# Optimization experiments

Measured on AMD Instinct MI355X. Metric: run time of the kernel, lower is better.

## Reference

```python
import jax, jax.numpy as jnp
import numpy as np

TOP_K = 2


def setup_inputs() -> dict:
    key = jax.random.key(0)
    k0, k1, k2, k3 = jax.random.split(key, 4)
    N, D, O, E = 131072, 512, 512, 16
    H = D // 4  # gate hidden: gate_input_size // 4
    x = jax.random.normal(k0, (N, D), dtype=jnp.float32)
    # gate MLP params (task_bh=0 gate; Linear weights stored as [in, out])
    Wg1 = jax.random.normal(k1, (D, H), dtype=jnp.float32) / np.sqrt(D).astype(np.float32)
    bg1 = jnp.zeros((H,), jnp.float32)
    Wg2 = jax.random.normal(k2, (H, E), dtype=jnp.float32) * 0.02
    bg2 = jnp.zeros((E,), jnp.float32)
    # per-expert Linear(D, O) weights stacked [E, D, O]
    We = jax.random.normal(k3, (E, D, O), dtype=jnp.float32) / np.sqrt(D).astype(np.float32)
    be = jnp.zeros((E, O), jnp.float32)
    return {"x": x, "Wg1": Wg1, "bg1": bg1, "Wg2": Wg2, "bg2": bg2,
            "We": We, "be": be, "task_bh": 0}


def reference(x, Wg1, bg1, Wg2, bg2, We, be, task_bh):
    # --- top_k_gating (noisy_gating=False path) ---
    h = jax.nn.gelu(x @ Wg1 + bg1, approximate=False)  # nn.GELU default is exact erf
    logits = h @ Wg2 + bg2                              # [N, E]
    probs = jax.nn.softmax(logits, axis=1) + 1e-4       # [N, E]
    top_g, top_i = jax.lax.top_k(probs, TOP_K)          # [N, K]
    N, E = probs.shape
    # dense gate matrix: zeros.scatter(1, top_k_indices, top_k_gates)
    gates = jnp.zeros_like(probs).at[jnp.arange(N)[:, None], top_i].set(top_g)
    # --- dispatch / per-expert GEMM / combine ---
    # Equivalent to: gather tokens per expert, expert Linear, scale by gate,
    # scatter-add back. Since gates[n, e] == 0 for unselected experts, the
    # combined output equals sum_e gates[:, e] * (x @ We[e] + be[e]).
    def body(acc, ewb):
        W_e, b_e, g_e = ewb                      # [D,O], [O], [N]
        return acc + g_e[:, None] * (x @ W_e + b_e), None
    init = jnp.zeros((N, We.shape[2]), x.dtype)
    out, _ = jax.lax.scan(body, init, (We, be, gates.T))
    return out
```

## Files before the change

kernel.cpp:

```cpp
#include <hip/hip_runtime.h>
#include <cstdint>
#include <math.h>


#define NTOK 131072
#define DDIM 512

typedef short  bf16x8 __attribute__((ext_vector_type(8)));
typedef float  f32x4  __attribute__((ext_vector_type(4)));

__device__ __forceinline__ ushort f2bf(float f){
  uint u = __float_as_uint(f);
  u += 0x7fffu + ((u >> 16) & 1u);
  return (ushort)(u >> 16);
}
__device__ __forceinline__ float bf2f(ushort h){ return __uint_as_float(((uint)h) << 16); }

__device__ __forceinline__ void load_lds16(const void* g, void* l){
  __builtin_amdgcn_global_load_lds(
      (const __attribute__((address_space(1))) void*)(uintptr_t)g,
      (__attribute__((address_space(3))) void*)(uintptr_t)l, 16, 0, 0);
}

__device__ __forceinline__ f32x4 MFMA(bf16x8 a, bf16x8 b, f32x4 c){
  return __builtin_amdgcn_mfma_f32_16x16x32_bf16(a, b, c, 0, 0, 0);
}

__device__ __forceinline__ bf16x8 readF64(const char* buf, int r, int q){
  return *(const bf16x8*)(buf + r*128 + ((q ^ (r & 7)) << 4));
}
__device__ __forceinline__ bf16x8 readF32c(const char* buf, int r, int q){
  return *(const bf16x8*)(buf + r*64 + ((q ^ (r & 3)) << 4));
}

__device__ __forceinline__ void stageB32(const ushort* grow, char* lds, int tid){
  const char* gb = (const char*)grow;
  #pragma unroll
  for (int i = 0; i < 2; ++i){
    int lin = i*4096 + tid*16;
    int r = lin >> 6;
    int g = (lin >> 4) & 3;
    load_lds16(gb + r*1024 + ((g ^ (r & 3)) << 4), lds + i*4096 + ((tid >> 6) << 10));
  }
}

__device__ __forceinline__ void pack8(const float* fv, uint* ph, uint* pl){
  #pragma unroll
  for (int q=0;q<4;++q){
    float f0 = fv[2*q], f1 = fv[2*q+1];
    ushort h0 = f2bf(f0), h1 = f2bf(f1);
    ushort s0 = f2bf(f0 - bf2f(h0)), s1 = f2bf(f1 - bf2f(h1));
    ph[q] = (uint)h0 | ((uint)h1 << 16);
    pl[q] = (uint)s0 | ((uint)s1 << 16);
  }
}
__device__ __forceinline__ void writeA2p(char* hbuf, char* lbuf, int ar, int acq,
                                         const uint* ph, const uint* pl){
  int off = ar*64 + ((acq ^ (ar & 3)) << 4);
  *(uint4*)(hbuf + off) = make_uint4(ph[0],ph[1],ph[2],ph[3]);
  *(uint4*)(lbuf + off) = make_uint4(pl[0],pl[1],pl[2],pl[3]);
}

__global__ void kconv(const float* __restrict__ We, const float* __restrict__ Wg1,
                      ushort* __restrict__ Wt, ushort* __restrict__ W1h, ushort* __restrict__ W1l){
  __shared__ float sh[64*65];
  int bx = blockIdx.x, tid = threadIdx.x;
  if (bx < 1024){
    int e = bx >> 6, dt = (bx >> 3) & 7, ot = bx & 7;
    const float* src = We + (size_t)e*262144 + (size_t)dt*64*512 + ot*64;
    #pragma unroll
    for (int it=0; it<16; ++it){ int idx = it*256+tid; int dl = idx>>6, ol = idx&63;
      sh[dl*65+ol] = src[dl*512+ol]; }
    __syncthreads();
    ushort* dst = Wt + (size_t)e*262144 + (size_t)ot*64*512 + dt*64;
    #pragma unroll
    for (int it=0; it<16; ++it){ int idx = it*256+tid; int ol = idx>>6, dl = idx&63;
      dst[(size_t)ol*512+dl] = f2bf(sh[dl*65+ol]); }
  } else {
    int q = bx - 1024;
    int dt = q >> 1, ht = q & 1;
    const float* src = Wg1 + (size_t)dt*64*128 + ht*64;
    #pragma unroll
    for (int it=0; it<16; ++it){ int idx = it*256+tid; int dl = idx>>6, ol = idx&63;
      sh[dl*65+ol] = src[dl*128+ol]; }
    __syncthreads();
    #pragma unroll
    for (int it=0; it<16; ++it){ int idx = it*256+tid; int ol = idx>>6, dl = idx&63;
      float wv = sh[dl*65+ol];
      ushort hi = f2bf(wv);
      ushort lo = f2bf(wv - bf2f(hi));
      size_t o = (size_t)(ht*64+ol)*512 + dt*64+dl;
      W1h[o] = hi; W1l[o] = lo; }
  }
}

__global__ __launch_bounds__(256) void kgate(
    const float* __restrict__ x, const ushort* __restrict__ W1h, const ushort* __restrict__ W1l,
    const float* __restrict__ bg1, const float* __restrict__ Wg2, const float* __restrict__ bg2,
    ushort* __restrict__ xbf,
    int2* __restrict__ gate_e, float2* __restrict__ gate_g,
    int* __restrict__ refine_cnt, int* __restrict__ refine_list, int* __restrict__ counts)
{
  __shared__ __align__(16) char sm[49152];
  const int BOFF = 16384;
  int tid = threadIdx.x, bid = blockIdx.x;
  int lane = tid & 63, w = tid >> 6, wm = w >> 1, wn = w & 1;
  int t0 = bid * 64;
  int ar = tid >> 2, acq = tid & 3;
  const float* xrow = x + (size_t)(t0 + ar) * DDIM;
  char* xbfb = (char*)xbf;
  f32x4 acc[2][4];
  #pragma unroll
  for (int n=0;n<4;++n){
    float bb = bg1[wn*64 + n*16 + (lane & 15)];
    f32x4 z = {bb, bb, bb, bb};
    acc[0][n] = z; acc[1][n] = z;
  }
  stageB32(W1h, sm + BOFF, tid);
  stageB32(W1l, sm + BOFF + 8192, tid);
  {
    float fv[8];
    *(float4*)&fv[0] = *(const float4*)(xrow + acq*8);
    *(float4*)&fv[4] = *(const float4*)(xrow + acq*8 + 4);
    uint ph[4], pl[4];
    pack8(fv, ph, pl);
    if (xbf) *(uint4*)(xbfb + (size_t)(t0+ar)*1024 + acq*16) = make_uint4(ph[0],ph[1],ph[2],ph[3]);
    writeA2p(sm, sm + 4096, ar, acq, ph, pl);
  }
  for (int ks = 0; ks < 16; ++ks){
    int b = ks & 1;
    asm volatile("s_waitcnt vmcnt(0)" ::: "memory");
    __syncthreads();
    uint ph[4], pl[4];
    if (ks < 15){
      int k2 = ks + 1, b2 = k2 & 1;
      stageB32(W1h + k2*32, sm + BOFF + b2*16384, tid);
      stageB32(W1l + k2*32, sm + BOFF + b2*16384 + 8192, tid);
      float fv[8];
      *(float4*)&fv[0] = *(const float4*)(xrow + k2*32 + acq*8);
      *(float4*)&fv[4] = *(const float4*)(xrow + k2*32 + acq*8 + 4);
      pack8(fv, ph, pl);
      if (xbf) *(uint4*)(xbfb + (size_t)(t0+ar)*1024 + k2*64 + acq*16) = make_uint4(ph[0],ph[1],ph[2],ph[3]);
    }
    const char* Ah = sm + b*8192;
    const char* Al = Ah + 4096;
    const char* Bh = sm + BOFF + b*16384;
    const char* Bl = Bh + 8192;
    bf16x8 ah[2], alv[2], bh[4], blv[4];
    #pragma unroll
    for (int m=0;m<2;++m){
      int r = wm*32 + m*16 + (lane & 15);
      ah[m]  = readF32c(Ah, r, lane >> 4);
      alv[m] = readF32c(Al, r, lane >> 4);
    }
    #pragma unroll
    for (int n=0;n<4;++n){
      int r = wn*64 + n*16 + (lane & 15);
      bh[n]  = readF32c(Bh, r, lane >> 4);
      blv[n] = readF32c(Bl, r, lane >> 4);
    }
    #pragma unroll
    for (int m=0;m<2;++m)
      #pragma unroll
      for (int n=0;n<4;++n){
        acc[m][n] = MFMA(ah[m],  bh[n],  acc[m][n]);
        acc[m][n] = MFMA(ah[m],  blv[n], acc[m][n]);
        acc[m][n] = MFMA(alv[m], bh[n],  acc[m][n]);
      }
    if (ks < 15){
      int b2 = (ks + 1) & 1;
      writeA2p(sm + b2*8192, sm + b2*8192 + 4096, ar, acq, ph, pl);
    }
  }
  __syncthreads();
  float* hl = (float*)sm;
  #pragma unroll
  for (int m=0;m<2;++m)
    #pragma unroll
    for (int n=0;n<4;++n)
      #pragma unroll
      for (int j=0;j<4;++j){
        int row = wm*32 + m*16 + ((lane >> 4) << 2) + j;
        int col = wn*64 + n*16 + (lane & 15);
        float uv = acc[m][n][j];
        hl[row*132 + col] = 0.5f * uv * (1.0f + erff(uv * 0.70710678118654752f));
      }
  __syncthreads();
  {
    int tt = tid >> 2, cc = tid & 3;
    float4 bb = *(const float4*)(bg2 + cc*4);
    float l0 = bb.x, l1 = bb.y, l2 = bb.z, l3 = bb.w;
    const float* hrow = hl + tt*132;
    #pragma unroll 8
    for (int i = 0; i < 128; ++i){
      float hv = hrow[i];
      float4 wv = *(const float4*)(Wg2 + i*16 + cc*4);
      l0 += hv*wv.x; l1 += hv*wv.y; l2 += hv*wv.z; l3 += hv*wv.w;
    }
    float* ll = (float*)(sm + 33792);
    *(float4*)(ll + tt*16 + cc*4) = make_float4(l0, l1, l2, l3);
  }
  int* hist = (int*)(sm + 40960);
  hist[tid] = 0;
  __syncthreads();
  if (tid < 64){
    int t = t0 + tid;
    const float* l = (const float*)(sm + 33792) + tid*16;
    float b1 = -1e30f, b2 = -1e30f, b3 = -1e30f; int e1 = 0, e2 = 0;
    #pragma unroll
    for (int e = 0; e < 16; ++e){
      float v = l[e];
      if (v > b1){ b3 = b2; b2 = b1; e2 = e1; b1 = v; e1 = e; }
      else if (v > b2){ b3 = b2; b2 = v; e2 = e; }
      else if (v > b3){ b3 = v; }
    }
    double s = 0.0;
    #pragma unroll
    for (int e = 0; e < 16; ++e) s += exp((double)l[e] - (double)b1);
    double inv = 1.0 / s;
    gate_e[t] = make_int2(e1, e2);
    gate_g[t] = make_float2((float)(inv + 1e-4), (float)(exp((double)b2 - (double)b1) * inv + 1e-4));
    if (b2 - b3 < 2e-4f){
      int pos = atomicAdd(refine_cnt, 1);
      refine_list[pos] = t;
    }
    int pa = min(e1, e2), pb = max(e1, e2);
    atomicAdd(&hist[pa*16 + pb], 1);
  }
  __syncthreads();
  if (hist[tid]) atomicAdd(&counts[tid], hist[tid]);
}

__global__ __launch_bounds__(128) void krefine(
    const float* __restrict__ x, const float* __restrict__ Wg1, const float* __restrict__ bg1,
    const float* __restrict__ Wg2, const float* __restrict__ bg2,
    const int* __restrict__ refine_cnt, const int* __restrict__ refine_list,
    int2* __restrict__ gate_e, float2* __restrict__ gate_g, int* __restrict__ counts)
{
  __shared__ float  xs[512];
  __shared__ double hd[128];
  __shared__ double ld[16];
  int tid = threadIdx.x;
  int rc = *refine_cnt;
  for (int i = blockIdx.x; i < rc; i += gridDim.x){
    __syncthreads();
    int t = refine_list[i];
    *(float4*)(xs + tid*4) = *(const float4*)(x + (size_t)t*DDIM + tid*4);
    __syncthreads();
    double a = (double)bg1[tid];
    for (int d = 0; d < 512; ++d) a += (double)xs[d] * (double)Wg1[d*128 + tid];
    hd[tid] = 0.5 * a * (1.0 + erf(a * 0.70710678118654752440));
    __syncthreads();
    if (tid < 16){
      double s = (double)bg2[tid];
      for (int k = 0; k < 128; ++k) s += hd[k] * (double)Wg2[k*16 + tid];
      ld[tid] = s;
    }
    __syncthreads();
    if (tid == 0){
      int2 olde = gate_e[t];
      double b1 = -1e300, b2 = -1e300; int e1 = 0, e2 = 0;
      for (int e = 0; e < 16; ++e){
        double v = ld[e];
        if (v > b1){ b2 = b1; e2 = e1; b1 = v; e1 = e; }
        else if (v > b2){ b2 = v; e2 = e; }
      }
      double s = 0.0;
      for (int e = 0; e < 16; ++e) s += exp(ld[e] - b1);
      double inv = 1.0 / s;
      int oldp = min(olde.x, olde.y)*16 + max(olde.x, olde.y);
      int newp = min(e1, e2)*16 + max(e1, e2);
      if (oldp != newp){ atomicSub(&counts[oldp], 1); atomicAdd(&counts[newp], 1); }
      gate_e[t] = make_int2(e1, e2);
      gate_g[t] = make_float2((float)(inv + 1e-4), (float)(exp(b2 - b1) * inv + 1e-4));
    }
  }
}

__global__ void kscan(const int* __restrict__ counts, int* __restrict__ bases,
                      int* __restrict__ tile_pair, int* __restrict__ tile_row0, int* __restrict__ ntiles){
  int l = threadIdx.x;
  int4 c = *(const int4*)(counts + l*4);
  int s = c.x + c.y + c.z + c.w;
  int ps = s;
  #pragma unroll
  for (int d = 1; d < 64; d <<= 1){ int v = __shfl_up(ps, d); if (l >= d) ps += v; }
  int ex = ps - s;
  bases[4*l+0] = ex;
  bases[4*l+1] = ex + c.x;
  bases[4*l+2] = ex + c.x + c.y;
  bases[4*l+3] = ex + c.x + c.y + c.z;
  if (l == 63) bases[256] = ex + s;
  int t0 = (c.x + 127) >> 7, t1 = (c.y + 127) >> 7, t2 = (c.z + 127) >> 7, t3 = (c.w + 127) >> 7;
  int ts = t0 + t1 + t2 + t3;
  int pt = ts;
  #pragma unroll
  for (int d = 1; d < 64; d <<= 1){ int v = __shfl_up(pt, d); if (l >= d) pt += v; }
  int ext = pt - ts;
  if (l == 63) *ntiles = ext + ts;
  int tb = ext;
  int cc[4] = {c.x, c.y, c.z, c.w};
  #pragma unroll
  for (int j = 0; j < 4; ++j){
    int pp = 4*l + j;
    for (int r = 0; r < cc[j]; r += 128){ tile_pair[tb] = pp; tile_row0[tb] = r; ++tb; }
  }
}

__global__ void kscatter(const int2* __restrict__ gate_e, const float2* __restrict__ gate_g,
                         const int* __restrict__ bases, int* __restrict__ cursors,
                         int* __restrict__ pair_tok, float2* __restrict__ pair_g){
  __shared__ int h[256];
  __shared__ int gb[256];
  int tid = threadIdx.x;
  h[tid] = 0; __syncthreads();
  int t = blockIdx.x*256 + tid;
  int2 ee = gate_e[t]; float2 gg = gate_g[t];
  int a, b; float ga, gbv;
  if (ee.x < ee.y){ a = ee.x; b = ee.y; ga = gg.x; gbv = gg.y; }
  else            { a = ee.y; b = ee.x; ga = gg.y; gbv = gg.x; }
  int p = a*16 + b;
  int off = atomicAdd(&h[p], 1);
  __syncthreads();
  if (h[tid]) gb[tid] = bases[tid] + atomicAdd(&cursors[tid], h[tid]);
  __syncthreads();
  int slot = gb[p] + off;
  pair_tok[slot] = t;
  pair_g[slot] = make_float2(ga, gbv);
}

template<int BF16A>
__global__ __launch_bounds__(256, 2) void kexpert(
    const float* __restrict__ x, const ushort* __restrict__ xbf,
    const ushort* __restrict__ Wt, const float* __restrict__ be,
    float* __restrict__ out,
    const int* __restrict__ counts, const int* __restrict__ bases,
    const int* __restrict__ tile_pair, const int* __restrict__ tile_row0, const int* __restrict__ ntiles,
    const int* __restrict__ pair_tok, const float2* __restrict__ pair_g)
{
  __shared__ __align__(16) char sm[67072];
  const int ABUF = 0, BBUF = 32768, LTOK = 65536, LGOFF = 66048;
  int tile = blockIdx.x >> 2, nt = blockIdx.x & 3;
  if (tile >= *ntiles) return;
  int p = tile_pair[tile], row0 = tile_row0[tile];
  int base = bases[p], cnt = counts[p];
  int eA = p >> 4, eB = p & 15;
  int tid = threadIdx.x, lane = tid & 63;
  int w = tid >> 6, wm = w >> 1, wn = w & 1;
  if (tid < 128){
    int rr = row0 + tid; bool v = rr < cnt;
    ((int*)(sm + LTOK))[tid] = v ? pair_tok[base + rr] : -1;
    ((float2*)(sm + LGOFF))[tid] = v ? pair_g[base + rr] : make_float2(0.f, 0.f);
  }
  __syncthreads();

  const char* wb = (const char*)Wt;
  int grp = tid >> 3;
  int gch = tid & 7;
  int sw  = (gch ^ (grp & 7)) << 4;
  long long edelt = ((long long)eB - (long long)eA) * 524288;
  const char* srcB[4];
  #pragma unroll
  for (int i = 0; i < 4; ++i)
    srcB[i] = wb + (long long)eA*524288 + (size_t)(nt*128 + i*32 + grp)*1024 + sw;

  const char* srcA[4];
  const float* xrow = nullptr; int arow = 0, ach = 0;
  if (BF16A){
    const char* xb = (const char*)xbf;
    #pragma unroll
    for (int i = 0; i < 4; ++i){
      int tk = ((const int*)(sm + LTOK))[i*32 + grp];
      if (tk < 0) tk = 0;
      srcA[i] = xb + (size_t)tk*1024 + sw;
    }
  } else {
    arow = tid >> 1; ach = tid & 1;
    int tk = ((const int*)(sm + LTOK))[arow];
    if (tk < 0) tk = 0;
    xrow = x + (size_t)tk*DDIM + ach*32;
  }
  int ldst = (w << 10);

  #pragma unroll
  for (int i = 0; i < 4; ++i){
    load_lds16(srcB[i], sm + BBUF + i*4096 + ldst);
    if (BF16A) load_lds16(srcA[i], sm + ABUF + i*4096 + ldst);
  }
  if (!BF16A){
    uint pk[16];
    #pragma unroll
    for (int q2 = 0; q2 < 4; ++q2){
      float4 fv = *(const float4*)(xrow + q2*8);
      float4 fw = *(const float4*)(xrow + q2*8 + 4);
      pk[q2*4+0] = (uint)f2bf(fv.x) | ((uint)f2bf(fv.y) << 16);
      pk[q2*4+1] = (uint)f2bf(fv.z) | ((uint)f2bf(fv.w) << 16);
      pk[q2*4+2] = (uint)f2bf(fw.x) | ((uint)f2bf(fw.y) << 16);
      pk[q2*4+3] = (uint)f2bf(fw.z) | ((uint)f2bf(fw.w) << 16);
    }
    #pragma unroll
    for (int q2 = 0; q2 < 4; ++q2){
      int g = ach*4 + q2;
      *(uint4*)(sm + ABUF + arow*128 + ((g ^ (arow & 7)) << 4)) =
          make_uint4(pk[q2*4], pk[q2*4+1], pk[q2*4+2], pk[q2*4+3]);
    }
  }

  f32x4 acc[4][4], res[4][4];
  #pragma unroll
  for (int m=0;m<4;++m)
    #pragma unroll
    for (int n=0;n<4;++n) acc[m][n] = (f32x4){0.f,0.f,0.f,0.f};

  for (int u = 0; u < 16; ++u){
    int b = u & 1;
    asm volatile("s_waitcnt vmcnt(0)" ::: "memory");
    __syncthreads();
    int un = u + 1;
    uint pk[16];
    if (un < 16){
      int b2 = un & 1;
      long long aoff = (long long)(un & 7) * 128;
      long long boff = aoff + ((un >> 3) ? edelt : 0);
      #pragma unroll
      for (int i = 0; i < 4; ++i){
        load_lds16(srcB[i] + boff, sm + BBUF + b2*16384 + i*4096 + ldst);
        if (BF16A) load_lds16(srcA[i] + aoff, sm + ABUF + b2*16384 + i*4096 + ldst);
      }
      if (!BF16A){
        const float* xr = xrow + (un & 7)*64;
        #pragma unroll
        for (int q2 = 0; q2 < 4; ++q2){
          float4 fv = *(const float4*)(xr + q2*8);
          float4 fw = *(const float4*)(xr + q2*8 + 4);
          pk[q2*4+0] = (uint)f2bf(fv.x) | ((uint)f2bf(fv.y) << 16);
          pk[q2*4+1] = (uint)f2bf(fv.z) | ((uint)f2bf(fv.w) << 16);
          pk[q2*4+2] = (uint)f2bf(fw.x) | ((uint)f2bf(fw.y) << 16);
          pk[q2*4+3] = (uint)f2bf(fw.z) | ((uint)f2bf(fw.w) << 16);
        }
      }
    }
    const char* Ab = sm + ABUF + b*16384;
    const char* Bb = sm + BBUF + b*16384;
    bf16x8 af[4][2], bf[4][2];
    #pragma unroll
    for (int m=0;m<4;++m){
      int r = wm*64 + m*16 + (lane & 15);
      af[m][0] = readF64(Ab, r, (lane >> 4));
      af[m][1] = readF64(Ab, r, 4 + (lane >> 4));
    }
    #pragma unroll
    for (int n=0;n<4;++n){
      int r = wn*64 + n*16 + (lane & 15);
      bf[n][0] = readF64(Bb, r, (lane >> 4));
      bf[n][1] = readF64(Bb, r, 4 + (lane >> 4));
    }
    #pragma unroll
    for (int m=0;m<4;++m)
      #pragma unroll
      for (int n=0;n<4;++n){
        acc[m][n] = MFMA(af[m][0], bf[n][0], acc[m][n]);
        acc[m][n] = MFMA(af[m][1], bf[n][1], acc[m][n]);
      }
    if (!BF16A && un < 16){
      int b2 = un & 1;
      #pragma unroll
      for (int q2 = 0; q2 < 4; ++q2){
        int g = ach*4 + q2;
        *(uint4*)(sm + ABUF + b2*16384 + arow*128 + ((g ^ (arow & 7)) << 4)) =
            make_uint4(pk[q2*4], pk[q2*4+1], pk[q2*4+2], pk[q2*4+3]);
      }
    }
    if (u == 7){
      const float* bev = be + (size_t)eA*DDIM + nt*128;
      float bcol[4];
      #pragma unroll
      for (int n=0;n<4;++n) bcol[n] = bev[wn*64 + n*16 + (lane & 15)];
      #pragma unroll
      for (int m=0;m<4;++m){
        #pragma unroll
        for (int j=0;j<4;++j){
          int row = wm*64 + m*16 + ((lane >> 4) << 2) + j;
          float g = ((const float2*)(sm + LGOFF))[row].x;
          #pragma unroll
          for (int n=0;n<4;++n){
            res[m][n][j] = g * (acc[m][n][j] + bcol[n]);
            acc[m][n][j] = 0.f;
          }
        }
      }
    }
    if (u == 15){
      const float* bev = be + (size_t)eB*DDIM + nt*128;
      float bcol[4];
      #pragma unroll
      for (int n=0;n<4;++n) bcol[n] = bev[wn*64 + n*16 + (lane & 15)];
      #pragma unroll
      for (int m=0;m<4;++m){
        #pragma unroll
        for (int j=0;j<4;++j){
          int row = wm*64 + m*16 + ((lane >> 4) << 2) + j;
          int tk = ((const int*)(sm + LTOK))[row];
          float g = ((const float2*)(sm + LGOFF))[row].y;
          if (tk >= 0){
            float* orow = out + (size_t)tk*DDIM + nt*128;
            #pragma unroll
            for (int n=0;n<4;++n)
              orow[wn*64 + n*16 + (lane & 15)] = res[m][n][j] + g * (acc[m][n][j] + bcol[n]);
          }
        }
      }
    }
  }
}

extern "C" void kernel_launch(void* const* d_in, const int* in_sizes, int n_in,
                              void* d_out, int out_size, void* d_ws, size_t ws_size,
                              hipStream_t stream)
{
  const float* x   = (const float*)d_in[0];
  const float* Wg1 = (const float*)d_in[1];
  const float* bg1 = (const float*)d_in[2];
  const float* Wg2 = (const float*)d_in[3];
  const float* bg2 = (const float*)d_in[4];
  const float* We  = (const float*)d_in[5];
  const float* be  = (const float*)d_in[6];
  float* out = (float*)d_out;
  char* ws = (char*)d_ws;

  ushort* Wt        = (ushort*)(ws + 0);
  ushort* W1h       = (ushort*)(ws + 8388608);
  ushort* W1l       = (ushort*)(ws + 8519680);
  char*   CTRL      = ws + 8650752;
  int*  refine_cnt  = (int*)(CTRL);
  int*  ntiles      = (int*)(CTRL + 4);
  int*  counts      = (int*)(CTRL + 64);
  int*  cursors     = (int*)(CTRL + 2048);
  int*  bases       = (int*)(CTRL + 4096);
  int2*   gate_e    = (int2*)(ws + 8658944);
  float2* gate_g    = (float2*)(ws + 9707520);
  int*  refine_list = (int*)(ws + 10756096);
  int*  pair_tok    = (int*)(ws + 11280384);
  float2* pair_g    = (float2*)(ws + 11804672);
  int*  tile_pair   = (int*)(ws + 12853248);
  int*  tile_row0   = (int*)(ws + 12863488);
  const size_t XBF_OFF = 16777216ull;
  const size_t XBF_BYTES = (size_t)NTOK * DDIM * 2;
  bool bf16a = ws_size >= XBF_OFF + XBF_BYTES;
  ushort* xbf = bf16a ? (ushort*)(ws + XBF_OFF) : nullptr;

  hipMemsetAsync(CTRL, 0, 8192, stream);
  hipLaunchKernelGGL(kconv,    dim3(1040), dim3(256), 0, stream, We, Wg1, Wt, W1h, W1l);
  hipLaunchKernelGGL(kgate,    dim3(2048), dim3(256), 0, stream, x, W1h, W1l, bg1, Wg2, bg2,
                     xbf, gate_e, gate_g, refine_cnt, refine_list, counts);
  hipLaunchKernelGGL(krefine,  dim3(512),  dim3(128), 0, stream, x, Wg1, bg1, Wg2, bg2,
                     refine_cnt, refine_list, gate_e, gate_g, counts);
  hipLaunchKernelGGL(kscan,    dim3(1),    dim3(64),  0, stream, counts, bases, tile_pair, tile_row0, ntiles);
  hipLaunchKernelGGL(kscatter, dim3(512),  dim3(256), 0, stream, gate_e, gate_g, bases, cursors, pair_tok, pair_g);
  if (bf16a)
    hipLaunchKernelGGL((kexpert<1>), dim3(5120), dim3(256), 0, stream, x, xbf, Wt, be, out,
                       counts, bases, tile_pair, tile_row0, ntiles, pair_tok, pair_g);
  else
    hipLaunchKernelGGL((kexpert<0>), dim3(5120), dim3(256), 0, stream, x, xbf, Wt, be, out,
                       counts, bases, tile_pair, tile_row0, ntiles, pair_tok, pair_g);
  (void)in_sizes; (void)n_in; (void)out_size; (void)ws_size;
}
```

Measured before the change: 488.1 us.

## Replace bf16 expert GEMM with 256x256-tile, 8-wave pipelined kernel

Adds kexpert2, a 512-thread kernel using 256-row by 256-column output tiles (scan tile size becomes 256), with double-buffered async LDS loads interleaved with MFMA phases and explicit barriers and setprio hints. Both experts are accumulated into a single accumulator by rescaling midway with the gate ratio, and the bias terms are applied at the end, so the second result buffer is no longer needed. The larger tile is meant to raise data reuse per LDS byte and cut redundant A/B loads. In exchange it pads more rows for small pairs, leaves fewer blocks per launch, and the g.x/g.y division risks precision loss when the second gate is tiny.

```diff
diff --git a/kernel.cpp b/kernel.cpp
--- a/kernel.cpp
+++ b/kernel.cpp
@@ -5,6 +5,7 @@
 
 #define NTOK 131072
 #define DDIM 512
+#define NT 16
 
 typedef short  bf16x8 __attribute__((ext_vector_type(8)));
 typedef float  f32x4  __attribute__((ext_vector_type(4)));
@@ -278,7 +279,8 @@
 }
 
 __global__ void kscan(const int* __restrict__ counts, int* __restrict__ bases,
-                      int* __restrict__ tile_pair, int* __restrict__ tile_row0, int* __restrict__ ntiles){
+                      int* __restrict__ tile_pair, int* __restrict__ tile_row0, int* __restrict__ ntiles,
+                      int ts){
   int l = threadIdx.x;
   int4 c = *(const int4*)(counts + l*4);
   int s = c.x + c.y + c.z + c.w;
@@ -291,19 +293,19 @@
   bases[4*l+2] = ex + c.x + c.y;
   bases[4*l+3] = ex + c.x + c.y + c.z;
   if (l == 63) bases[256] = ex + s;
-  int t0 = (c.x + 127) >> 7, t1 = (c.y + 127) >> 7, t2 = (c.z + 127) >> 7, t3 = (c.w + 127) >> 7;
-  int ts = t0 + t1 + t2 + t3;
-  int pt = ts;
+  int t0 = (c.x + ts-1) / ts, t1 = (c.y + ts-1) / ts, t2 = (c.z + ts-1) / ts, t3 = (c.w + ts-1) / ts;
+  int tsum = t0 + t1 + t2 + t3;
+  int pt = tsum;
   #pragma unroll
   for (int d = 1; d < 64; d <<= 1){ int v = __shfl_up(pt, d); if (l >= d) pt += v; }
-  int ext = pt - ts;
-  if (l == 63) *ntiles = ext + ts;
+  int ext = pt - tsum;
+  if (l == 63) *ntiles = ext + tsum;
   int tb = ext;
   int cc[4] = {c.x, c.y, c.z, c.w};
   #pragma unroll
   for (int j = 0; j < 4; ++j){
     int pp = 4*l + j;
-    for (int r = 0; r < cc[j]; r += 128){ tile_pair[tb] = pp; tile_row0[tb] = r; ++tb; }
+    for (int r = 0; r < cc[j]; r += ts){ tile_pair[tb] = pp; tile_row0[tb] = r; ++tb; }
   }
 }
 
@@ -329,9 +331,163 @@
   pair_g[slot] = make_float2(ga, gbv);
 }
 
-template<int BF16A>
-__global__ __launch_bounds__(256, 2) void kexpert(
-    const float* __restrict__ x, const ushort* __restrict__ xbf,
+#define SBAR0 __builtin_amdgcn_sched_barrier(0)
+#define BARR  do{ asm volatile("" ::: "memory"); SBAR0; __builtin_amdgcn_s_barrier(); SBAR0; asm volatile("" ::: "memory"); }while(0)
+
+#define RDA(hp, mb) do{ \
+  _Pragma("unroll") for (int m_=0;m_<4;++m_){ \
+    int r_ = ((mb)+m_)*16 + l15; \
+    af[m_][0] = readF64(hp, r_, l4); \
+    af[m_][1] = readF64(hp, r_, 4+l4); }}while(0)
+#define RDB(hp, bv, nb) do{ \
+  _Pragma("unroll") for (int n_=0;n_<2;++n_){ \
+    int r_ = bln + ((nb)+n_)*16 + l15; \
+    bv[n_][0] = readF64(hp, r_, l4); \
+    bv[n_][1] = readF64(hp, r_, 4+l4); }}while(0)
+#define MMAC(bv, mb, nb) do{ \
+  __builtin_amdgcn_s_setprio(1); \
+  _Pragma("unroll") for (int m_=0;m_<4;++m_){ \
+    _Pragma("unroll") for (int n_=0;n_<2;++n_){ \
+      acc[(mb)+m_][(nb)+n_] = MFMA(af[m_][0], bv[n_][0], acc[(mb)+m_][(nb)+n_]); \
+      acc[(mb)+m_][(nb)+n_] = MFMA(af[m_][1], bv[n_][1], acc[(mb)+m_][(nb)+n_]); }} \
+  __builtin_amdgcn_s_setprio(0); \
+}while(0)
+
+__global__ __launch_bounds__(512, 2) void kexpert2(
+    const ushort* __restrict__ xbf, const ushort* __restrict__ Wt, const float* __restrict__ be,
+    float* __restrict__ out,
+    const int* __restrict__ counts, const int* __restrict__ bases,
+    const int* __restrict__ tile_pair, const int* __restrict__ tile_row0, const int* __restrict__ ntiles,
+    const int* __restrict__ pair_tok, const float2* __restrict__ pair_g)
+{
+  __shared__ __align__(16) char sm[134144];
+  const int BBASE = 65536, LTOK = 131072, LG = 132096;
+  int bid = blockIdx.x;
+  int tile = ((bid >> 4) << 3) | (bid & 7);
+  int nt = (bid >> 3) & 1;
+  if (tile >= *ntiles) return;
+  int p = tile_pair[tile], row0 = tile_row0[tile];
+  int base = bases[p], cnt = counts[p];
+  int eA = p >> 4, eB = p & 15;
+  int tid = threadIdx.x, lane = tid & 63, w = tid >> 6;
+  int wm = w >> 2, wn = w & 3;
+  int l15 = lane & 15, l4 = lane >> 4;
+  int bln = (wn & 1) * 64;
+  if (tid < 256){
+    int rr = row0 + tid; bool v = rr < cnt;
+    ((int*)(sm + LTOK))[tid] = v ? pair_tok[base + rr] : -1;
+    ((float2*)(sm + LG))[tid] = v ? pair_g[base + rr] : make_float2(0.f, 1.f);
+  }
+  __syncthreads();
+
+  int rr0 = tid >> 3;
+  int sw = ((tid & 7) ^ (rr0 & 7)) << 4;
+  const char* xb = (const char*)xbf;
+  const char* srcA[2][2];
+  #pragma unroll
+  for (int h = 0; h < 2; ++h)
+    #pragma unroll
+    for (int i = 0; i < 2; ++i){
+      int tk = ((const int*)(sm + LTOK))[h*128 + i*64 + rr0];
+      if (tk < 0) tk = 0;
+      srcA[h][i] = xb + (size_t)tk*1024 + sw;
+    }
+  const char* srcB0 = (const char*)Wt + (size_t)eA*524288 + (size_t)(nt*256 + rr0)*1024 + sw;
+  long long edelt = ((long long)eB - eA) * 524288;
+  char* dA = sm + w*1024;
+  char* dB = sm + BBASE + w*1024;
+
+  auto stA = [&](int t, int h){
+    if (t >= NT) return;
+    int ks = t & 7, bf_ = t & 1;
+    load_lds16(srcA[h][0] + ks*128, dA + bf_*32768 + h*16384);
+    load_lds16(srcA[h][1] + ks*128, dA + bf_*32768 + h*16384 + 8192);
+  };
+  auto stB = [&](int t, int h){
+    if (t >= NT) return;
+    int ks = t & 7, bf_ = t & 1;
+    long long eo = ((t >= 8) ? edelt : 0) + ks*128;
+    load_lds16(srcB0 + h*131072 + eo,         dB + bf_*32768 + h*16384);
+    load_lds16(srcB0 + h*131072 + 65536 + eo, dB + bf_*32768 + h*16384 + 8192);
+  };
+
+  const char* A0 = sm + wm*16384;
+  const char* A1 = A0 + 32768;
+  const char* B0 = sm + BBASE + (wn >> 1)*16384;
+  const char* B1 = B0 + 32768;
+
+  f32x4 acc[8][4];
+  #pragma unroll
+  for (int m = 0; m < 8; ++m)
+    #pragma unroll
+    for (int n = 0; n < 4; ++n) acc[m][n] = (f32x4){0.f,0.f,0.f,0.f};
+
+  stA(0,0); stA(0,1); stB(0,0); stB(0,1); stB(1,0); stB(1,1);
+  asm volatile("s_waitcnt vmcnt(4)" ::: "memory");
+  BARR;
+
+  bf16x8 af[4][2], bL[2][2], bH[2][2];
+  #pragma unroll 1
+  for (int i = 0; i < 8; ++i){
+    int t0 = 2*i, t1 = t0 + 1;
+    RDA(A0, 0); RDB(B0, bL, 0); stA(t1, 0);
+    BARR; MMAC(bL, 0, 0); BARR;
+    RDB(B0, bH, 2); stA(t1, 1);
+    BARR; MMAC(bH, 0, 2); BARR;
+    RDA(A0, 4); stB(t0+2, 0);
+    BARR; MMAC(bH, 4, 2); BARR;
+    stB(t0+2, 1);
+    if (i != 7) { asm volatile("s_waitcnt vmcnt(4)" ::: "memory"); }
+    else        { asm volatile("s_waitcnt vmcnt(0)" ::: "memory"); }
+    BARR; MMAC(bL, 4, 0); BARR;
+    RDA(A1, 0); RDB(B1, bL, 0); stA(t0+2, 0);
+    BARR; MMAC(bL, 0, 0); BARR;
+    RDB(B1, bH, 2); stA(t0+2, 1);
+    BARR; MMAC(bH, 0, 2); BARR;
+    RDA(A1, 4); stB(t1+2, 0);
+    BARR; MMAC(bH, 4, 2); BARR;
+    stB(t1+2, 1);
+    if (i != 7) { asm volatile("s_waitcnt vmcnt(4)" ::: "memory"); }
+    BARR; MMAC(bL, 4, 0); BARR;
+    if (i == 3){
+      #pragma unroll
+      for (int m = 0; m < 8; ++m)
+        #pragma unroll
+        for (int j = 0; j < 4; ++j){
+          int row = wm*128 + m*16 + l4*4 + j;
+          float2 g2 = ((const float2*)(sm + LG))[row];
+          float r_ = g2.x / g2.y;
+          #pragma unroll
+          for (int n = 0; n < 4; ++n) acc[m][n][j] *= r_;
+        }
+    }
+  }
+
+  float bcA[4], bcB[4];
+  #pragma unroll
+  for (int n = 0; n < 4; ++n){
+    int col = nt*256 + wn*64 + n*16 + l15;
+    bcA[n] = be[(size_t)eA*DDIM + col];
+    bcB[n] = be[(size_t)eB*DDIM + col];
+  }
+  #pragma unroll
+  for (int m = 0; m < 8; ++m)
+    #pragma unroll
+    for (int j = 0; j < 4; ++j){
+      int row = wm*128 + m*16 + l4*4 + j;
+      int tk = ((const int*)(sm + LTOK))[row];
+      if (tk >= 0){
+        float2 g2 = ((const float2*)(sm + LG))[row];
+        float* orow = out + (size_t)tk*DDIM + nt*256 + wn*64;
+        #pragma unroll
+        for (int n = 0; n < 4; ++n)
+          orow[n*16 + l15] = g2.y*acc[m][n][j] + g2.x*bcA[n] + g2.y*bcB[n];
+      }
+    }
+}
+
+__global__ __launch_bounds__(256, 2) void kexpertF(
+    const float* __restrict__ x,
     const ushort* __restrict__ Wt, const float* __restrict__ be,
     float* __restrict__ out,
     const int* __restrict__ counts, const int* __restrict__ bases,
@@ -353,41 +509,22 @@
     ((float2*)(sm + LGOFF))[tid] = v ? pair_g[base + rr] : make_float2(0.f, 0.f);
   }
   __syncthreads();
-
   const char* wb = (const char*)Wt;
-  int grp = tid >> 3;
-  int gch = tid & 7;
-  int sw  = (gch ^ (grp & 7)) << 4;
+  int grp = tid >> 3, gch = tid & 7;
+  int swz = (gch ^ (grp & 7)) << 4;
   long long edelt = ((long long)eB - (long long)eA) * 524288;
   const char* srcB[4];
   #pragma unroll
   for (int i = 0; i < 4; ++i)
-    srcB[i] = wb + (long long)eA*524288 + (size_t)(nt*128 + i*32 + grp)*1024 + sw;
-
-  const char* srcA[4];
-  const float* xrow = nullptr; int arow = 0, ach = 0;
-  if (BF16A){
-    const char* xb = (const char*)xbf;
-    #pragma unroll
-    for (int i = 0; i < 4; ++i){
-      int tk = ((const int*)(sm + LTOK))[i*32 + grp];
-      if (tk < 0) tk = 0;
-      srcA[i] = xb + (size_t)tk*1024 + sw;
-    }
-  } else {
-    arow = tid >> 1; ach = tid & 1;
-    int tk = ((const int*)(sm + LTOK))[arow];
-    if (tk < 0) tk = 0;
-    xrow = x + (size_t)tk*DDIM + ach*32;
-  }
+    srcB[i] = wb + (long long)eA*524288 + (size_t)(nt*128 + i*32 + grp)*1024 + swz;
+  int arow = tid >> 1, ach = tid & 1;
+  int tkr = ((const int*)(sm + LTOK))[arow];
+  if (tkr < 0) tkr = 0;
+  const float* xrow = x + (size_t)tkr*DDIM + ach*32;
   int ldst = (w << 10);
-
-  #pragma unroll
-  for (int i = 0; i < 4; ++i){
-    load_lds16(srcB[i], sm + BBUF + i*4096 + ldst);
-    if (BF16A) load_lds16(srcA[i], sm + ABUF + i*4096 + ldst);
-  }
-  if (!BF16A){
+  #pragma unroll
+  for (int i = 0; i < 4; ++i) load_lds16(srcB[i], sm + BBUF + i*4096 + ldst);
+  {
     uint pk[16];
     #pragma unroll
     for (int q2 = 0; q2 < 4; ++q2){
@@ -405,13 +542,11 @@
           make_uint4(pk[q2*4], pk[q2*4+1], pk[q2*4+2], pk[q2*4+3]);
     }
   }
-
   f32x4 acc[4][4], res[4][4];
   #pragma unroll
   for (int m=0;m<4;++m)
     #pragma unroll
     for (int n=0;n<4;++n) acc[m][n] = (f32x4){0.f,0.f,0.f,0.f};
-
   for (int u = 0; u < 16; ++u){
     int b = u & 1;
     asm volatile("s_waitcnt vmcnt(0)" ::: "memory");
@@ -423,46 +558,42 @@
       long long aoff = (long long)(un & 7) * 128;
       long long boff = aoff + ((un >> 3) ? edelt : 0);
       #pragma unroll
-      for (int i = 0; i < 4; ++i){
+      for (int i = 0; i < 4; ++i)
         load_lds16(srcB[i] + boff, sm + BBUF + b2*16384 + i*4096 + ldst);
-        if (BF16A) load_lds16(srcA[i] + aoff, sm + ABUF + b2*16384 + i*4096 + ldst);
-      }
-      if (!BF16A){
-        const float* xr = xrow + (un & 7)*64;
-        #pragma unroll
-        for (int q2 = 0; q2 < 4; ++q2){
-          float4 fv = *(const float4*)(xr + q2*8);
-          float4 fw = *(const float4*)(xr + q2*8 + 4);
-          pk[q2*4+0] = (uint)f2bf(fv.x) | ((uint)f2bf(fv.y) << 16);
-          pk[q2*4+1] = (uint)f2bf(fv.z) | ((uint)f2bf(fv.w) << 16);
-          pk[q2*4+2] = (uint)f2bf(fw.x) | ((uint)f2bf(fw.y) << 16);
-          pk[q2*4+3] = (uint)f2bf(fw.z) | ((uint)f2bf(fw.w) << 16);
-        }
+      const float* xr = xrow + (un & 7)*64;
+      #pragma unroll
+      for (int q2 = 0; q2 < 4; ++q2){
+        float4 fv = *(const float4*)(xr + q2*8);
+        float4 fw = *(const float4*)(xr + q2*8 + 4);
+        pk[q2*4+0] = (uint)f2bf(fv.x) | ((uint)f2bf(fv.y) << 16);
+        pk[q2*4+1] = (uint)f2bf(fv.z) | ((uint)f2bf(fv.w) << 16);
+        pk[q2*4+2] = (uint)f2bf(fw.x) | ((uint)f2bf(fw.y) << 16);
+        pk[q2*4+3] = (uint)f2bf(fw.z) | ((uint)f2bf(fw.w) << 16);
       }
     }
     const char* Ab = sm + ABUF + b*16384;
     const char* Bb = sm + BBUF + b*16384;
-    bf16x8 af[4][2], bf[4][2];
+    bf16x8 af2[4][2], bf2[4][2];
     #pragma unroll
     for (int m=0;m<4;++m){
       int r = wm*64 + m*16 + (lane & 15);
-      af[m][0] = readF64(Ab, r, (lane >> 4));
-      af[m][1] = readF64(Ab, r, 4 + (lane >> 4));
+      af2[m][0] = readF64(Ab, r, (lane >> 4));
+      af2[m][1] = readF64(Ab, r, 4 + (lane >> 4));
     }
     #pragma unroll
     for (int n=0;n<4;++n){
       int r = wn*64 + n*16 + (lane & 15);
-      bf[n][0] = readF64(Bb, r, (lane >> 4));
-      bf[n][1] = readF64(Bb, r, 4 + (lane >> 4));
+      bf2[n][0] = readF64(Bb, r, (lane >> 4));
+      bf2[n][1] = readF64(Bb, r, 4 + (lane >> 4));
     }
     #pragma unroll
     for (int m=0;m<4;++m)
       #pragma unroll
       for (int n=0;n<4;++n){
-        acc[m][n] = MFMA(af[m][0], bf[n][0], acc[m][n]);
-        acc[m][n] = MFMA(af[m][1], bf[n][1], acc[m][n]);
+        acc[m][n] = MFMA(af2[m][0], bf2[n][0], acc[m][n]);
+        acc[m][n] = MFMA(af2[m][1], bf2[n][1], acc[m][n]);
       }
-    if (!BF16A && un < 16){
+    if (un < 16){
       int b2 = un & 1;
       #pragma unroll
       for (int q2 = 0; q2 < 4; ++q2){
@@ -477,7 +608,7 @@
       #pragma unroll
       for (int n=0;n<4;++n) bcol[n] = bev[wn*64 + n*16 + (lane & 15)];
       #pragma unroll
-      for (int m=0;m<4;++m){
+      for (int m=0;m<4;++m)
         #pragma unroll
         for (int j=0;j<4;++j){
           int row = wm*64 + m*16 + ((lane >> 4) << 2) + j;
@@ -488,7 +619,6 @@
             acc[m][n][j] = 0.f;
           }
         }
-      }
     }
     if (u == 15){
       const float* bev = be + (size_t)eB*DDIM + nt*128;
@@ -496,7 +626,7 @@
       #pragma unroll
       for (int n=0;n<4;++n) bcol[n] = bev[wn*64 + n*16 + (lane & 15)];
       #pragma unroll
-      for (int m=0;m<4;++m){
+      for (int m=0;m<4;++m)
         #pragma unroll
         for (int j=0;j<4;++j){
           int row = wm*64 + m*16 + ((lane >> 4) << 2) + j;
@@ -509,7 +639,6 @@
               orow[wn*64 + n*16 + (lane & 15)] = res[m][n][j] + g * (acc[m][n][j] + bcol[n]);
           }
         }
-      }
     }
   }
 }
@@ -555,13 +684,14 @@
                      xbf, gate_e, gate_g, refine_cnt, refine_list, counts);
   hipLaunchKernelGGL(krefine,  dim3(512),  dim3(128), 0, stream, x, Wg1, bg1, Wg2, bg2,
                      refine_cnt, refine_list, gate_e, gate_g, counts);
-  hipLaunchKernelGGL(kscan,    dim3(1),    dim3(64),  0, stream, counts, bases, tile_pair, tile_row0, ntiles);
+  hipLaunchKernelGGL(kscan,    dim3(1),    dim3(64),  0, stream, counts, bases, tile_pair, tile_row0, ntiles,
+                     bf16a ? 256 : 128);
   hipLaunchKernelGGL(kscatter, dim3(512),  dim3(256), 0, stream, gate_e, gate_g, bases, cursors, pair_tok, pair_g);
   if (bf16a)
-    hipLaunchKernelGGL((kexpert<1>), dim3(5120), dim3(256), 0, stream, x, xbf, Wt, be, out,
+    hipLaunchKernelGGL(kexpert2, dim3(1408), dim3(512), 0, stream, xbf, Wt, be, out,
                        counts, bases, tile_pair, tile_row0, ntiles, pair_tok, pair_g);
   else
-    hipLaunchKernelGGL((kexpert<0>), dim3(5120), dim3(256), 0, stream, x, xbf, Wt, be, out,
+    hipLaunchKernelGGL(kexpertF, dim3(5120), dim3(256), 0, stream, x, Wt, be, out,
                        counts, bases, tile_pair, tile_row0, ntiles, pair_tok, pair_g);
   (void)in_sizes; (void)n_in; (void)out_size; (void)ws_size;
 }
```

Measured after the change: 446.3 us. 8.6% less time.
